# Kernel optimization log

Hardware: AMD Instinct MI355X
Metric: run time of the kernel (lower is better)

## Reference

```python
import jax, jax.numpy as jnp
import numpy as np

B, D, H, E = 32768, 128, 512, 16

def setup_inputs() -> dict:
    key = jax.random.key(0)
    ks = jax.random.split(key, 5)
    x = jax.random.normal(ks[0], (B, 1, D), dtype=jnp.float32)
    s1 = 1.0 / float(np.sqrt(H))   # init_ uses last-dim size: w1 last dim = H
    s2 = 1.0 / float(np.sqrt(D))   # w2 last dim = D
    sg = 1.0 / float(np.sqrt(D))   # nn.Linear(D, E) default init scale
    w1 = jax.random.uniform(ks[1], (E, D, H), minval=-s1, maxval=s1, dtype=jnp.float32)
    w2 = jax.random.uniform(ks[2], (E, H, D), minval=-s2, maxval=s2, dtype=jnp.float32)
    wg = jax.random.uniform(ks[3], (D, E), minval=-sg, maxval=sg, dtype=jnp.float32)
    bg = jax.random.uniform(ks[4], (E,), minval=-sg, maxval=sg, dtype=jnp.float32)
    return {"x": x, "w1": w1, "w2": w2, "wg": wg, "bg": bg}

def reference(x, w1, w2, wg, bg):
    xt = x[:, 0, :]                                   # (B, D); seq dim is 1 by construction
    logits = xt @ wg + bg                             # (B, E)
    topk_vals, topk_idx = jax.lax.top_k(logits, 1)    # (B, 1) each
    scores = jax.nn.softmax(topk_vals, axis=-1)       # (B, 1); all ones for k=1
    # every expert processes every token (faithful to the reference)
    hidden = jax.nn.gelu(jnp.einsum('bd,edh->ebh', xt, w1), approximate=False)  # (E, B, H)
    eout = jnp.einsum('ebh,ehd->ebd', hidden, w2)     # (E, B, D)
    # gather selected expert per token, scale, sum over k
    sel = jnp.take_along_axis(eout.transpose(1, 0, 2), topk_idx[:, :, None], axis=1)  # (B, 1, D)
    return (sel * scores[:, :, None]).sum(axis=1)     # (B, D)
```

## Files before the change

### kernel.cpp

```cpp
#include <hip/hip_runtime.h>
#include <hip/hip_bf16.h>
#include <math.h>

#define NB 32768
#define DD 128
#define HH 512
#define EE 16
#define TM 64

typedef __attribute__((ext_vector_type(8))) short short8;
typedef __attribute__((ext_vector_type(4))) float f32x4;

__device__ __forceinline__ unsigned short f2bf(float f) {
  union { float f; unsigned u; } v; v.f = f;
  unsigned r = v.u + 0x7fffu + ((v.u >> 16) & 1u);
  return (unsigned short)(r >> 16);
}

__device__ __forceinline__ float fast_erf(float z) {
  float a = fabsf(z);
  float t = 1.0f / (1.0f + 0.3275911f * a);
  float y = t * (0.254829592f + t * (-0.284496736f + t * (1.421413741f +
            t * (-1.453152027f + t * 1.061405429f))));
  float r = 1.0f - y * __expf(-a * a);
  return z < 0.0f ? -r : r;
}

__global__ __launch_bounds__(256) void transpose_kernel(
    const float* __restrict__ w1, const float* __restrict__ w2,
    unsigned short* __restrict__ w1T, unsigned short* __restrict__ w2T) {
  __shared__ float tile[32][33];
  int b = blockIdx.x;
  int tx = threadIdx.x & 31, ty = threadIdx.x >> 5;
  if (b < 1024) {
    int e = b >> 6, t = b & 63;
    int d0 = (t >> 4) * 32, h0 = (t & 15) * 32;
    const float* src = w1 + (size_t)e * DD * HH;
    #pragma unroll
    for (int j = 0; j < 4; ++j)
      tile[ty + j * 8][tx] = src[(size_t)(d0 + ty + j * 8) * HH + h0 + tx];
    __syncthreads();
    unsigned short* dst = w1T + (size_t)e * HH * DD;
    #pragma unroll
    for (int j = 0; j < 4; ++j)
      dst[(size_t)(h0 + ty + j * 8) * DD + d0 + tx] = f2bf(tile[tx][ty + j * 8]);
  } else {
    int bb = b - 1024;
    int e = bb >> 6, t = bb & 63;
    int h0 = (t >> 2) * 32, d0 = (t & 3) * 32;
    const float* src = w2 + (size_t)e * HH * DD;
    #pragma unroll
    for (int j = 0; j < 4; ++j)
      tile[ty + j * 8][tx] = src[(size_t)(h0 + ty + j * 8) * DD + d0 + tx];
    __syncthreads();
    unsigned short* dst = w2T + (size_t)e * DD * HH;
    #pragma unroll
    for (int j = 0; j < 4; ++j)
      dst[(size_t)(d0 + ty + j * 8) * HH + h0 + tx] = f2bf(tile[tx][ty + j * 8]);
  }
}

__global__ __launch_bounds__(256) void gate_kernel(
    const float* __restrict__ x, const float* __restrict__ wg,
    const float* __restrict__ bg, int* __restrict__ counts,
    int* __restrict__ rows) {
  __shared__ float sx[64][132];
  __shared__ double swg[DD][EE];
  __shared__ int lcnt[EE];
  __shared__ int gbase[EE];
  __shared__ int lslot[64];
  __shared__ int lexp[64];

  int tid = threadIdx.x;
  int base = blockIdx.x * 64;

  if (tid < EE) lcnt[tid] = 0;
  for (int i = tid; i < DD * EE; i += 256) swg[i >> 4][i & 15] = (double)wg[i];
  {
    int r = tid >> 2, c0 = (tid & 3) * 32;
    const float4* src = (const float4*)(x + (size_t)(base + r) * DD + c0);
    #pragma unroll
    for (int i = 0; i < 8; ++i)
      *(float4*)&sx[r][c0 + i * 4] = src[i];
  }
  __syncthreads();

  int r = tid >> 2;
  int e0 = (tid & 3) * 4;
  double acc[4];
  #pragma unroll
  for (int j = 0; j < 4; ++j) acc[j] = (double)bg[e0 + j];

  #pragma unroll 4
  for (int d = 0; d < DD; ++d) {
    double xv = (double)sx[r][d];
    #pragma unroll
    for (int j = 0; j < 4; ++j)
      acc[j] += xv * swg[d][e0 + j];
  }

  int beste = 0; double bestv = acc[0];
  #pragma unroll
  for (int j = 1; j < 4; ++j)
    if (acc[j] > bestv) { bestv = acc[j]; beste = j; }
  int ge = e0 + beste;

  #pragma unroll
  for (int off = 1; off < 4; off <<= 1) {
    double ov = __shfl_xor(bestv, off);
    int oe = __shfl_xor(ge, off);
    if (ov > bestv || (ov == bestv && oe < ge)) { bestv = ov; ge = oe; }
  }

  if ((tid & 3) == 0) {
    lslot[r] = atomicAdd(&lcnt[ge], 1);
    lexp[r] = ge;
  }
  __syncthreads();
  if (tid < EE && lcnt[tid] > 0)
    gbase[tid] = atomicAdd(&counts[tid], lcnt[tid]);
  __syncthreads();
  if ((tid & 3) == 0) {
    int e2 = lexp[r];
    rows[e2 * NB + gbase[e2] + lslot[r]] = base + r;
  }
}

__global__ __launch_bounds__(256) void moe_gemm(
    const float* __restrict__ x, const unsigned short* __restrict__ w1T,
    const unsigned short* __restrict__ w2T, const int* __restrict__ counts,
    const int* __restrict__ rows, float* __restrict__ out) {
  int e = blockIdx.y;
  int cnt = counts[e];
  int base = blockIdx.x * TM;
  if (base >= cnt) return;

  __shared__ unsigned short sX[TM][136];
  __shared__ unsigned short sW1[64][136];
  __shared__ unsigned short sW2[DD][72];
  __shared__ unsigned short sH[TM][72];

  int tid = threadIdx.x;
  {
    int m = tid >> 2;
    int c0 = (tid & 3) * 32;
    int ridx = base + m; if (ridx >= cnt) ridx = cnt - 1;
    int grow = rows[e * NB + ridx];
    const float4* src = (const float4*)(x + (size_t)grow * DD + c0);
    #pragma unroll
    for (int i = 0; i < 8; ++i) {
      float4 v = src[i];
      ushort4 p;
      p.x = f2bf(v.x); p.y = f2bf(v.y); p.z = f2bf(v.z); p.w = f2bf(v.w);
      *(ushort4*)&sX[m][c0 + i * 4] = p;
    }
  }

  int wv = tid >> 6;
  int l  = tid & 63;
  int lm = l & 15;
  int q  = l >> 4;
  int k0 = q * 8;

  f32x4 acc2[8];
  #pragma unroll
  for (int n = 0; n < 8; ++n) acc2[n] = (f32x4){0.f, 0.f, 0.f, 0.f};

  for (int hc = 0; hc < HH / 64; ++hc) {
    int h0 = hc * 64;
    {
      const uint4* src = (const uint4*)(w1T + ((size_t)e * HH + h0) * DD);
      #pragma unroll
      for (int i = 0; i < 4; ++i) {
        int u = tid + i * 256;
        int r = u >> 4, c = u & 15;
        *(uint4*)&sW1[r][c * 8] = src[u];
      }
    }
    {
      #pragma unroll
      for (int i = 0; i < 4; ++i) {
        int u = tid + i * 256;
        int r = u >> 3, c = u & 7;
        const uint4* src = (const uint4*)(w2T + ((size_t)e * DD + r) * HH + h0);
        *(uint4*)&sW2[r][c * 8] = src[c];
      }
    }
    __syncthreads();

    f32x4 acc1[4];
    #pragma unroll
    for (int n = 0; n < 4; ++n) acc1[n] = (f32x4){0.f, 0.f, 0.f, 0.f};
    #pragma unroll
    for (int ks = 0; ks < 4; ++ks) {
      int kk = ks * 32 + k0;
      short8 a = *(const short8*)&sX[wv * 16 + lm][kk];
      #pragma unroll
      for (int n = 0; n < 4; ++n) {
        short8 bfr = *(const short8*)&sW1[n * 16 + lm][kk];
        acc1[n] = __builtin_amdgcn_mfma_f32_16x16x32_bf16(a, bfr, acc1[n], 0, 0, 0);
      }
    }
    #pragma unroll
    for (int n = 0; n < 4; ++n) {
      #pragma unroll
      for (int r = 0; r < 4; ++r) {
        float v = acc1[n][r];
        float g = 0.5f * v * (1.0f + fast_erf(v * 0.70710678118654752f));
        sH[wv * 16 + q * 4 + r][n * 16 + lm] = f2bf(g);
      }
    }
    __syncthreads();

    #pragma unroll
    for (int ks = 0; ks < 2; ++ks) {
      int kk = ks * 32 + k0;
      short8 a = *(const short8*)&sH[wv * 16 + lm][kk];
      #pragma unroll
      for (int n = 0; n < 8; ++n) {
        short8 bfr = *(const short8*)&sW2[n * 16 + lm][kk];
        acc2[n] = __builtin_amdgcn_mfma_f32_16x16x32_bf16(a, bfr, acc2[n], 0, 0, 0);
      }
    }
    __syncthreads();
  }

  #pragma unroll
  for (int r = 0; r < 4; ++r) {
    int ml = wv * 16 + q * 4 + r;
    int ridx = base + ml;
    if (ridx < cnt) {
      int grow = rows[e * NB + ridx];
      float* op = out + (size_t)grow * DD + lm;
      #pragma unroll
      for (int n = 0; n < 8; ++n) op[n * 16] = acc2[n][r];
    }
  }
}

extern "C" void kernel_launch(void* const* d_in, const int* in_sizes, int n_in,
                              void* d_out, int out_size, void* d_ws, size_t ws_size,
                              hipStream_t stream) {
  const float* x  = (const float*)d_in[0];
  const float* w1 = (const float*)d_in[1];
  const float* w2 = (const float*)d_in[2];
  const float* wg = (const float*)d_in[3];
  const float* bg = (const float*)d_in[4];
  float* out = (float*)d_out;

  int* counts = (int*)d_ws;
  int* rows   = (int*)((char*)d_ws + 1024);
  unsigned short* w1T = (unsigned short*)((char*)d_ws + 1024 + (size_t)EE * NB * 4);
  unsigned short* w2T = w1T + (size_t)EE * HH * DD;

  hipMemsetAsync(d_ws, 0, 64, stream);
  hipLaunchKernelGGL(transpose_kernel, dim3(2048), dim3(256), 0, stream, w1, w2, w1T, w2T);
  hipLaunchKernelGGL(gate_kernel, dim3(NB / 64), dim3(256), 0, stream, x, wg, bg, counts, rows);
  hipLaunchKernelGGL(moe_gemm, dim3(NB / TM, EE), dim3(256), 0, stream, x, w1T, w2T, counts, rows, out);
}
```

Baseline: 143.0 us.

## Prefetch expert weight chunks into registers and reorder the MoE grid by expert

The MoE GEMM now loads the next 64-wide hidden chunk of W1 and W2 into registers while the current chunk is computed, then stores it to shared memory after a barrier. This overlaps global-memory latency with MFMA work. The barrier between writing and reading the GELU tile is dropped, because each wave only reads the rows it wrote itself. The grid is transposed so the expert index varies fastest, which spreads the few non-empty row tiles of every expert across the early dispatch instead of scheduling long runs of empty blocks per expert. The cost is extra register pressure from the prefetch buffers.

```diff
diff --git a/kernel.cpp b/kernel.cpp
--- a/kernel.cpp
+++ b/kernel.cpp
@@ -130,9 +130,9 @@
     const float* __restrict__ x, const unsigned short* __restrict__ w1T,
     const unsigned short* __restrict__ w2T, const int* __restrict__ counts,
     const int* __restrict__ rows, float* __restrict__ out) {
-  int e = blockIdx.y;
+  int e = blockIdx.x;
   int cnt = counts[e];
-  int base = blockIdx.x * TM;
+  int base = blockIdx.y * TM;
   if (base >= cnt) return;
 
   __shared__ unsigned short sX[TM][136];
@@ -162,32 +162,40 @@
   int q  = l >> 4;
   int k0 = q * 8;
 
+  uint4 pf1[4], pf2[4];
+  const uint4* w1base = (const uint4*)(w1T + (size_t)e * HH * DD);
+
+  #pragma unroll
+  for (int i = 0; i < 4; ++i) pf1[i] = w1base[tid + i * 256];
+  #pragma unroll
+  for (int i = 0; i < 4; ++i) {
+    int u = tid + i * 256, r2 = u >> 3, c2 = u & 7;
+    pf2[i] = *(const uint4*)(w2T + ((size_t)e * DD + r2) * HH + c2 * 8);
+  }
+  #pragma unroll
+  for (int i = 0; i < 4; ++i) {
+    int u = tid + i * 256, r2 = u >> 4, c2 = u & 15;
+    *(uint4*)&sW1[r2][c2 * 8] = pf1[i];
+  }
+  #pragma unroll
+  for (int i = 0; i < 4; ++i) {
+    int u = tid + i * 256, r2 = u >> 3, c2 = u & 7;
+    *(uint4*)&sW2[r2][c2 * 8] = pf2[i];
+  }
+  #pragma unroll
+  for (int i = 0; i < 4; ++i) pf1[i] = w1base[1024 + tid + i * 256];
+  #pragma unroll
+  for (int i = 0; i < 4; ++i) {
+    int u = tid + i * 256, r2 = u >> 3, c2 = u & 7;
+    pf2[i] = *(const uint4*)(w2T + ((size_t)e * DD + r2) * HH + 64 + c2 * 8);
+  }
+  __syncthreads();
+
   f32x4 acc2[8];
   #pragma unroll
   for (int n = 0; n < 8; ++n) acc2[n] = (f32x4){0.f, 0.f, 0.f, 0.f};
 
-  for (int hc = 0; hc < HH / 64; ++hc) {
-    int h0 = hc * 64;
-    {
-      const uint4* src = (const uint4*)(w1T + ((size_t)e * HH + h0) * DD);
-      #pragma unroll
-      for (int i = 0; i < 4; ++i) {
-        int u = tid + i * 256;
-        int r = u >> 4, c = u & 15;
-        *(uint4*)&sW1[r][c * 8] = src[u];
-      }
-    }
-    {
-      #pragma unroll
-      for (int i = 0; i < 4; ++i) {
-        int u = tid + i * 256;
-        int r = u >> 3, c = u & 7;
-        const uint4* src = (const uint4*)(w2T + ((size_t)e * DD + r) * HH + h0);
-        *(uint4*)&sW2[r][c * 8] = src[c];
-      }
-    }
-    __syncthreads();
-
+  for (int hc = 0; hc < 8; ++hc) {
     f32x4 acc1[4];
     #pragma unroll
     for (int n = 0; n < 4; ++n) acc1[n] = (f32x4){0.f, 0.f, 0.f, 0.f};
@@ -210,8 +218,6 @@
         sH[wv * 16 + q * 4 + r][n * 16 + lm] = f2bf(g);
       }
     }
-    __syncthreads();
-
     #pragma unroll
     for (int ks = 0; ks < 2; ++ks) {
       int kk = ks * 32 + k0;
@@ -222,7 +228,30 @@
         acc2[n] = __builtin_amdgcn_mfma_f32_16x16x32_bf16(a, bfr, acc2[n], 0, 0, 0);
       }
     }
-    __syncthreads();
+    if (hc < 7) {
+      __syncthreads();
+      #pragma unroll
+      for (int i = 0; i < 4; ++i) {
+        int u = tid + i * 256, r2 = u >> 4, c2 = u & 15;
+        *(uint4*)&sW1[r2][c2 * 8] = pf1[i];
+      }
+      #pragma unroll
+      for (int i = 0; i < 4; ++i) {
+        int u = tid + i * 256, r2 = u >> 3, c2 = u & 7;
+        *(uint4*)&sW2[r2][c2 * 8] = pf2[i];
+      }
+      if (hc < 6) {
+        int h0n = (hc + 2) * 64;
+        #pragma unroll
+        for (int i = 0; i < 4; ++i) pf1[i] = w1base[(size_t)(hc + 2) * 1024 + tid + i * 256];
+        #pragma unroll
+        for (int i = 0; i < 4; ++i) {
+          int u = tid + i * 256, r2 = u >> 3, c2 = u & 7;
+          pf2[i] = *(const uint4*)(w2T + ((size_t)e * DD + r2) * HH + h0n + c2 * 8);
+        }
+      }
+      __syncthreads();
+    }
   }
 
   #pragma unroll
@@ -256,5 +285,5 @@
   hipMemsetAsync(d_ws, 0, 64, stream);
   hipLaunchKernelGGL(transpose_kernel, dim3(2048), dim3(256), 0, stream, w1, w2, w1T, w2T);
   hipLaunchKernelGGL(gate_kernel, dim3(NB / 64), dim3(256), 0, stream, x, wg, bg, counts, rows);
-  hipLaunchKernelGGL(moe_gemm, dim3(NB / TM, EE), dim3(256), 0, stream, x, w1T, w2T, counts, rows, out);
-}
+  hipLaunchKernelGGL(moe_gemm, dim3(EE, NB / TM), dim3(256), 0, stream, x, w1T, w2T, counts, rows, out);
+}
```

New measurement: 164.9 us. 1.15x slower.

## Merge prep kernels, double-buffer weight chunks, keep X in registers, swizzle LDS

Applied to the files above, without the earlier changes.

Merges the weight transpose and gate/routing into one prep kernel, so one launch is dropped. The transpose now uses 64x64 tiles with vectorized loads and stores. The MoE GEMM shrinks the hidden chunk to 32, double-buffers the W1/W2 chunks in LDS with register prefetch of the next chunk, and keeps the bf16 X fragments in registers instead of LDS. XOR swizzling replaces padding to avoid bank conflicts. The grid is reordered so that experts vary fastest, which may change L2 reuse of weights. Smaller chunks mean more loop iterations and barriers per tile.

```diff
diff --git a/kernel.cpp b/kernel.cpp
--- a/kernel.cpp
+++ b/kernel.cpp
@@ -7,6 +7,8 @@
 #define HH 512
 #define EE 16
 #define TM 64
+#define HC 32
+#define NCH (HH / HC)
 
 typedef __attribute__((ext_vector_type(8))) short short8;
 typedef __attribute__((ext_vector_type(4))) float f32x4;
@@ -26,54 +28,58 @@
   return z < 0.0f ? -r : r;
 }
 
-__global__ __launch_bounds__(256) void transpose_kernel(
-    const float* __restrict__ w1, const float* __restrict__ w2,
-    unsigned short* __restrict__ w1T, unsigned short* __restrict__ w2T) {
-  __shared__ float tile[32][33];
-  int b = blockIdx.x;
-  int tx = threadIdx.x & 31, ty = threadIdx.x >> 5;
-  if (b < 1024) {
-    int e = b >> 6, t = b & 63;
-    int d0 = (t >> 4) * 32, h0 = (t & 15) * 32;
-    const float* src = w1 + (size_t)e * DD * HH;
-    #pragma unroll
-    for (int j = 0; j < 4; ++j)
-      tile[ty + j * 8][tx] = src[(size_t)(d0 + ty + j * 8) * HH + h0 + tx];
+__global__ __launch_bounds__(256) void prep_kernel(
+    const float* __restrict__ x, const float* __restrict__ wg,
+    const float* __restrict__ bg, const float* __restrict__ w1,
+    const float* __restrict__ w2, int* __restrict__ counts,
+    int* __restrict__ rows, unsigned short* __restrict__ w1T,
+    unsigned short* __restrict__ w2T) {
+  __shared__ __align__(16) char smem[50816];
+  int tid = threadIdx.x;
+
+  if (blockIdx.x >= 512) {
+    float (*tile)[65] = (float (*)[65])smem;
+    int tp = blockIdx.x - 512;
+    const float* src; unsigned short* dst; int S, Sd;
+    if (tp < 256) {
+      int e = tp >> 4, t2 = tp & 15;
+      int d0 = (t2 >> 3) * 64, h0 = (t2 & 7) * 64;
+      src = w1 + (size_t)e * DD * HH + (size_t)d0 * HH + h0; S = HH;
+      dst = w1T + (size_t)e * HH * DD + (size_t)h0 * DD + d0; Sd = DD;
+    } else {
+      int t = tp - 256;
+      int e = t >> 4, t2 = t & 15;
+      int h0 = (t2 >> 1) * 64, d0 = (t2 & 1) * 64;
+      src = w2 + (size_t)e * HH * DD + (size_t)h0 * DD + d0; S = DD;
+      dst = w2T + (size_t)e * DD * HH + (size_t)d0 * HH + h0; Sd = HH;
+    }
+    #pragma unroll
+    for (int i = 0; i < 4; ++i) {
+      int u = tid + i * 256, r = u >> 4, c = (u & 15) * 4;
+      float4 v = *(const float4*)(src + (size_t)r * S + c);
+      tile[r][c + 0] = v.x; tile[r][c + 1] = v.y;
+      tile[r][c + 2] = v.z; tile[r][c + 3] = v.w;
+    }
     __syncthreads();
-    unsigned short* dst = w1T + (size_t)e * HH * DD;
-    #pragma unroll
-    for (int j = 0; j < 4; ++j)
-      dst[(size_t)(h0 + ty + j * 8) * DD + d0 + tx] = f2bf(tile[tx][ty + j * 8]);
-  } else {
-    int bb = b - 1024;
-    int e = bb >> 6, t = bb & 63;
-    int h0 = (t >> 2) * 32, d0 = (t & 3) * 32;
-    const float* src = w2 + (size_t)e * HH * DD;
-    #pragma unroll
-    for (int j = 0; j < 4; ++j)
-      tile[ty + j * 8][tx] = src[(size_t)(h0 + ty + j * 8) * DD + d0 + tx];
-    __syncthreads();
-    unsigned short* dst = w2T + (size_t)e * DD * HH;
-    #pragma unroll
-    for (int j = 0; j < 4; ++j)
-      dst[(size_t)(d0 + ty + j * 8) * HH + h0 + tx] = f2bf(tile[tx][ty + j * 8]);
-  }
-}
-
-__global__ __launch_bounds__(256) void gate_kernel(
-    const float* __restrict__ x, const float* __restrict__ wg,
-    const float* __restrict__ bg, int* __restrict__ counts,
-    int* __restrict__ rows) {
-  __shared__ float sx[64][132];
-  __shared__ double swg[DD][EE];
-  __shared__ int lcnt[EE];
-  __shared__ int gbase[EE];
-  __shared__ int lslot[64];
-  __shared__ int lexp[64];
-
-  int tid = threadIdx.x;
+    #pragma unroll
+    for (int i = 0; i < 4; ++i) {
+      int u = tid + i * 256, tr = u >> 4, tc = (u & 15) * 4;
+      ushort4 p;
+      p.x = f2bf(tile[tc + 0][tr]); p.y = f2bf(tile[tc + 1][tr]);
+      p.z = f2bf(tile[tc + 2][tr]); p.w = f2bf(tile[tc + 3][tr]);
+      *(ushort4*)(dst + (size_t)tr * Sd + tc) = p;
+    }
+    return;
+  }
+
+  float  (*sx)[132] = (float (*)[132])smem;
+  double (*swg)[EE] = (double (*)[EE])(smem + 33792);
+  int* lcnt  = (int*)(smem + 50176);
+  int* gbase = lcnt + EE;
+  int* lslot = gbase + EE;
+  int* lexp  = lslot + 64;
+
   int base = blockIdx.x * 64;
-
   if (tid < EE) lcnt[tid] = 0;
   for (int i = tid; i < DD * EE; i += 256) swg[i >> 4][i & 15] = (double)wg[i];
   {
@@ -130,110 +136,127 @@
     const float* __restrict__ x, const unsigned short* __restrict__ w1T,
     const unsigned short* __restrict__ w2T, const int* __restrict__ counts,
     const int* __restrict__ rows, float* __restrict__ out) {
-  int e = blockIdx.y;
+  int e = blockIdx.x;
   int cnt = counts[e];
-  int base = blockIdx.x * TM;
+  int base = blockIdx.y * TM;
   if (base >= cnt) return;
 
-  __shared__ unsigned short sX[TM][136];
-  __shared__ unsigned short sW1[64][136];
-  __shared__ unsigned short sW2[DD][72];
-  __shared__ unsigned short sH[TM][72];
+  __shared__ unsigned short sW1[2][HC][DD];
+  __shared__ unsigned short sW2[2][DD][HC];
+  __shared__ unsigned short sH[TM][HC];
 
   int tid = threadIdx.x;
+  int wv = tid >> 6, l = tid & 63;
+  int lm = l & 15, q = l >> 4;
+
+  short8 xa[4];
   {
-    int m = tid >> 2;
-    int c0 = (tid & 3) * 32;
-    int ridx = base + m; if (ridx >= cnt) ridx = cnt - 1;
+    int ridx = base + wv * 16 + lm; if (ridx >= cnt) ridx = cnt - 1;
     int grow = rows[e * NB + ridx];
-    const float4* src = (const float4*)(x + (size_t)grow * DD + c0);
-    #pragma unroll
-    for (int i = 0; i < 8; ++i) {
-      float4 v = src[i];
-      ushort4 p;
-      p.x = f2bf(v.x); p.y = f2bf(v.y); p.z = f2bf(v.z); p.w = f2bf(v.w);
-      *(ushort4*)&sX[m][c0 + i * 4] = p;
-    }
-  }
-
-  int wv = tid >> 6;
-  int l  = tid & 63;
-  int lm = l & 15;
-  int q  = l >> 4;
-  int k0 = q * 8;
+    const float* xr = x + (size_t)grow * DD + q * 8;
+    #pragma unroll
+    for (int ks = 0; ks < 4; ++ks) {
+      f32x4 v0 = *(const f32x4*)(xr + ks * 32);
+      f32x4 v1 = *(const f32x4*)(xr + ks * 32 + 4);
+      short8 a;
+      a[0] = f2bf(v0[0]); a[1] = f2bf(v0[1]); a[2] = f2bf(v0[2]); a[3] = f2bf(v0[3]);
+      a[4] = f2bf(v1[0]); a[5] = f2bf(v1[1]); a[6] = f2bf(v1[2]); a[7] = f2bf(v1[3]);
+      xa[ks] = a;
+    }
+  }
+
+  int r1s = tid >> 4, s1s = tid & 15;
+  int sl1 = (s1s ^ (r1s & 7)) * 8;
+  int r2s = tid >> 2, s2s = tid & 3;
+  int sl2 = (s2s ^ ((r2s >> 1) & 3)) * 8;
+
+  {
+    const unsigned short* w1c = w1T + (size_t)e * HH * DD;
+    const unsigned short* w2c = w2T + (size_t)e * DD * HH;
+    uint4 a0 = *(const uint4*)(w1c + (size_t)tid * 8);
+    uint4 a1 = *(const uint4*)(w1c + (size_t)(tid + 256) * 8);
+    uint4 b0 = *(const uint4*)(w2c + (size_t)r2s * HH + s2s * 8);
+    uint4 b1 = *(const uint4*)(w2c + (size_t)(r2s + 64) * HH + s2s * 8);
+    *(uint4*)&sW1[0][r1s][sl1]      = a0;
+    *(uint4*)&sW1[0][r1s + 16][sl1] = a1;
+    *(uint4*)&sW2[0][r2s][sl2]      = b0;
+    *(uint4*)&sW2[0][r2s + 64][sl2] = b1;
+  }
+  __syncthreads();
 
   f32x4 acc2[8];
   #pragma unroll
   for (int n = 0; n < 8; ++n) acc2[n] = (f32x4){0.f, 0.f, 0.f, 0.f};
 
-  for (int hc = 0; hc < HH / 64; ++hc) {
-    int h0 = hc * 64;
+  for (int hc = 0; hc < NCH; ++hc) {
+    int b = hc & 1;
+
+    uint4 pa0, pa1, pb0, pb1;
+    if (hc + 1 < NCH) {
+      const unsigned short* w1c = w1T + ((size_t)e * HH + (size_t)(hc + 1) * HC) * DD;
+      const unsigned short* w2c = w2T + (size_t)e * DD * HH + (size_t)(hc + 1) * HC;
+      pa0 = *(const uint4*)(w1c + (size_t)tid * 8);
+      pa1 = *(const uint4*)(w1c + (size_t)(tid + 256) * 8);
+      pb0 = *(const uint4*)(w2c + (size_t)r2s * HH + s2s * 8);
+      pb1 = *(const uint4*)(w2c + (size_t)(r2s + 64) * HH + s2s * 8);
+    }
+
+    f32x4 acc1[2];
+    #pragma unroll
+    for (int n = 0; n < 2; ++n) acc1[n] = (f32x4){0.f, 0.f, 0.f, 0.f};
+    #pragma unroll
+    for (int ks = 0; ks < 4; ++ks) {
+      #pragma unroll
+      for (int n = 0; n < 2; ++n) {
+        int row = n * 16 + lm;
+        int sl = ((ks * 4 + q) ^ (row & 7)) * 8;
+        short8 bfr = *(const short8*)&sW1[b][row][sl];
+        acc1[n] = __builtin_amdgcn_mfma_f32_16x16x32_bf16(xa[ks], bfr, acc1[n], 0, 0, 0);
+      }
+    }
+    #pragma unroll
+    for (int n = 0; n < 2; ++n) {
+      #pragma unroll
+      for (int rr = 0; rr < 4; ++rr) {
+        float v = acc1[n][rr];
+        float g = 0.5f * v * (1.0f + fast_erf(v * 0.70710678118654752f));
+        int row = wv * 16 + q * 4 + rr;
+        int col = n * 16 + lm;
+        int sl = ((col >> 3) ^ ((row >> 1) & 3)) * 8;
+        sH[row][sl + (col & 7)] = f2bf(g);
+      }
+    }
     {
-      const uint4* src = (const uint4*)(w1T + ((size_t)e * HH + h0) * DD);
-      #pragma unroll
-      for (int i = 0; i < 4; ++i) {
-        int u = tid + i * 256;
-        int r = u >> 4, c = u & 15;
-        *(uint4*)&sW1[r][c * 8] = src[u];
-      }
-    }
-    {
-      #pragma unroll
-      for (int i = 0; i < 4; ++i) {
-        int u = tid + i * 256;
-        int r = u >> 3, c = u & 7;
-        const uint4* src = (const uint4*)(w2T + ((size_t)e * DD + r) * HH + h0);
-        *(uint4*)&sW2[r][c * 8] = src[c];
-      }
-    }
-    __syncthreads();
-
-    f32x4 acc1[4];
-    #pragma unroll
-    for (int n = 0; n < 4; ++n) acc1[n] = (f32x4){0.f, 0.f, 0.f, 0.f};
-    #pragma unroll
-    for (int ks = 0; ks < 4; ++ks) {
-      int kk = ks * 32 + k0;
-      short8 a = *(const short8*)&sX[wv * 16 + lm][kk];
-      #pragma unroll
-      for (int n = 0; n < 4; ++n) {
-        short8 bfr = *(const short8*)&sW1[n * 16 + lm][kk];
-        acc1[n] = __builtin_amdgcn_mfma_f32_16x16x32_bf16(a, bfr, acc1[n], 0, 0, 0);
-      }
-    }
-    #pragma unroll
-    for (int n = 0; n < 4; ++n) {
-      #pragma unroll
-      for (int r = 0; r < 4; ++r) {
-        float v = acc1[n][r];
-        float g = 0.5f * v * (1.0f + fast_erf(v * 0.70710678118654752f));
-        sH[wv * 16 + q * 4 + r][n * 16 + lm] = f2bf(g);
-      }
-    }
-    __syncthreads();
-
-    #pragma unroll
-    for (int ks = 0; ks < 2; ++ks) {
-      int kk = ks * 32 + k0;
-      short8 a = *(const short8*)&sH[wv * 16 + lm][kk];
+      int rowA = wv * 16 + lm;
+      int slA = (q ^ ((rowA >> 1) & 3)) * 8;
+      short8 a = *(const short8*)&sH[rowA][slA];
       #pragma unroll
       for (int n = 0; n < 8; ++n) {
-        short8 bfr = *(const short8*)&sW2[n * 16 + lm][kk];
+        int row = n * 16 + lm;
+        int sl = (q ^ ((row >> 1) & 3)) * 8;
+        short8 bfr = *(const short8*)&sW2[b][row][sl];
         acc2[n] = __builtin_amdgcn_mfma_f32_16x16x32_bf16(a, bfr, acc2[n], 0, 0, 0);
       }
     }
+
+    if (hc + 1 < NCH) {
+      *(uint4*)&sW1[b ^ 1][r1s][sl1]      = pa0;
+      *(uint4*)&sW1[b ^ 1][r1s + 16][sl1] = pa1;
+      *(uint4*)&sW2[b ^ 1][r2s][sl2]      = pb0;
+      *(uint4*)&sW2[b ^ 1][r2s + 64][sl2] = pb1;
+    }
     __syncthreads();
   }
 
   #pragma unroll
-  for (int r = 0; r < 4; ++r) {
-    int ml = wv * 16 + q * 4 + r;
+  for (int rr = 0; rr < 4; ++rr) {
+    int ml = wv * 16 + q * 4 + rr;
     int ridx = base + ml;
     if (ridx < cnt) {
       int grow = rows[e * NB + ridx];
       float* op = out + (size_t)grow * DD + lm;
       #pragma unroll
-      for (int n = 0; n < 8; ++n) op[n * 16] = acc2[n][r];
+      for (int n = 0; n < 8; ++n) op[n * 16] = acc2[n][rr];
     }
   }
 }
@@ -254,7 +277,8 @@
   unsigned short* w2T = w1T + (size_t)EE * HH * DD;
 
   hipMemsetAsync(d_ws, 0, 64, stream);
-  hipLaunchKernelGGL(transpose_kernel, dim3(2048), dim3(256), 0, stream, w1, w2, w1T, w2T);
-  hipLaunchKernelGGL(gate_kernel, dim3(NB / 64), dim3(256), 0, stream, x, wg, bg, counts, rows);
-  hipLaunchKernelGGL(moe_gemm, dim3(NB / TM, EE), dim3(256), 0, stream, x, w1T, w2T, counts, rows, out);
-}
+  hipLaunchKernelGGL(prep_kernel, dim3(1024), dim3(256), 0, stream,
+                     x, wg, bg, w1, w2, counts, rows, w1T, w2T);
+  hipLaunchKernelGGL(moe_gemm, dim3(EE, NB / TM), dim3(256), 0, stream,
+                     x, w1T, w2T, counts, rows, out);
+}
```

After: 135.6 us. 5.1% less time.
